# Kernel tuning notes

Measured on AMD Instinct MI355X. Metric: run time of the kernel, lower is better.

## Reference

```python
import jax, jax.numpy as jnp
import numpy as np

C = 512
NUM_HEADS = 8
RF = 4          # reduction_factor
GROUPS = 8      # min(8, C//8)
EPS = 1e-5


def _pos_enc(h, w, c):
    # matches torch _create_positional_encoding; c must be divisible by 4
    y = jnp.arange(h, dtype=jnp.float32)[:, None] * jnp.ones((1, w), jnp.float32)
    x = jnp.ones((h, 1), jnp.float32) * jnp.arange(w, dtype=jnp.float32)[None, :]
    div = jnp.exp(jnp.arange(0, c // 2, 2, dtype=jnp.float32) * (-np.log(10000.0) / (c // 2)))  # [c//4]
    d = div[:, None, None]
    sy, cy = jnp.sin(y[None] * d), jnp.cos(y[None] * d)   # [c//4,h,w]
    sx, cx = jnp.sin(x[None] * d), jnp.cos(x[None] * d)
    pe = jnp.stack([sy, cy, sx, cx], axis=1).reshape(c, h, w)  # interleaved 0::4..3::4
    return pe[None] * 0.01


def _group_norm(x, w, b):
    B, Cc, H, W = x.shape
    g = x.reshape(B, GROUPS, -1)
    m = g.mean(-1, keepdims=True)
    v = g.var(-1, keepdims=True)
    g = (g - m) / jnp.sqrt(v + EPS)
    return g.reshape(B, Cc, H, W) * w[None, :, None, None] + b[None, :, None, None]


def setup_inputs() -> dict:
    key = jax.random.key(0)
    ks = jax.random.split(key, 4)
    B, H, W = 1, 256, 256
    x = jax.random.normal(ks[0], (B, C, H, W), jnp.float32)
    qkv_w = jax.random.normal(ks[1], (3 * C, C), jnp.float32) * 0.02
    proj_w = jax.random.normal(ks[2], (C, C), jnp.float32) * 0.02
    gamma = jax.random.normal(ks[3], (1,), jnp.float32)
    return {
        "x": x,
        "gn_weight": jnp.ones((C,), jnp.float32),
        "gn_bias": jnp.zeros((C,), jnp.float32),
        "qkv_w": qkv_w,
        "proj_w": proj_w,
        "proj_b": jnp.zeros((C,), jnp.float32),
        "gamma": gamma,
        "temperature": jnp.ones((NUM_HEADS, 1, 1), jnp.float32),
    }


def reference(x, gn_weight, gn_bias, qkv_w, proj_w, proj_b, gamma, temperature):
    B, Cc, H, W = x.shape
    hd = Cc // NUM_HEADS
    identity = x
    xn = _group_norm(x, gn_weight, gn_bias)
    # spatial reduction (AvgPool2d k=4 s=4); H,W > 32 in this config
    Hr, Wr = H // RF, W // RF
    xr = xn.reshape(B, Cc, Hr, RF, Wr, RF).mean(axis=(3, 5))
    xr = xr + _pos_enc(Hr, Wr, Cc)
    qkv = jnp.einsum('oc,bchw->bohw', qkv_w, xr)  # 1x1 conv, no bias
    q, k, v = jnp.split(qkv, 3, axis=1)
    N = Hr * Wr
    q = q.reshape(B, NUM_HEADS, hd, N) * (hd ** -0.5) * temperature[None]
    k = k.reshape(B, NUM_HEADS, hd, N)
    v = v.reshape(B, NUM_HEADS, hd, N)
    # chunked attention in torch == plain softmax attention (chunking over queries)
    attn = jax.nn.softmax(jnp.einsum('bhdn,bhdm->bhnm', q, k), axis=-1)
    out = jnp.einsum('bhnm,bhdm->bhdn', attn, v).reshape(B, Cc, Hr, Wr)
    out = jax.image.resize(out, (B, Cc, H, W), method='bilinear')  # align_corners=False
    out = jnp.einsum('oc,bchw->bohw', proj_w, out) + proj_b[None, :, None, None]
    # dropout in eval mode is identity
    return identity + gamma * out
```

## Files before the change

### kernel.cpp

```cpp
#include <hip/hip_runtime.h>
#include <hip/hip_bf16.h>


typedef __attribute__((ext_vector_type(4))) short short4v;
typedef __attribute__((ext_vector_type(8))) short short8v;
typedef __attribute__((ext_vector_type(4))) float f32x4;
typedef __attribute__((ext_vector_type(4))) unsigned int u32x4;

#define MFMA16(a, b, c) __builtin_amdgcn_mfma_f32_16x16x32_bf16(a, b, c, 0, 0, 0)

__device__ __forceinline__ unsigned short bf16r(float f) {
    unsigned int u = __builtin_bit_cast(unsigned int, f);
    u += 0x7fffu + ((u >> 16) & 1u);
    return (unsigned short)(u >> 16);
}
__device__ __forceinline__ float bff(unsigned short s) {
    unsigned int u = ((unsigned int)s) << 16;
    return __builtin_bit_cast(float, u);
}
__device__ __forceinline__ unsigned int fbits(float f) {
    return __builtin_bit_cast(unsigned int, f);
}

typedef const __attribute__((address_space(1))) unsigned int guint;
typedef __attribute__((address_space(3))) unsigned int luint;
__device__ __forceinline__ void gload16(const void* g, void* l) {
    __builtin_amdgcn_global_load_lds((guint*)g, (luint*)l, 16, 0, 0);
}

__global__ __launch_bounds__(256) void k_wconv(const float* __restrict__ qkv_w,
                                               const float* __restrict__ proj_w,
                                               const float* __restrict__ temp,
                                               unsigned short* __restrict__ wq_b,
                                               unsigned short* __restrict__ wp_b) {
    int idx = blockIdx.x * 256 + threadIdx.x;
    const int NQ = 1536 * 512;
    if (idx < NQ) {
        int o = idx >> 9;
        float sc = (o < 512) ? temp[o >> 6] * 0.125f * 1.44269504f : 1.0f;
        wq_b[idx] = bf16r(qkv_w[idx] * sc);
    } else {
        int j = idx - NQ;
        wp_b[j] = bf16r(proj_w[j]);
    }
}

__global__ __launch_bounds__(256) void k_pool(const float* __restrict__ x,
                                              float* __restrict__ xp,
                                              float* __restrict__ partials) {
    int hr = blockIdx.x;
    int c  = blockIdx.y;
    int t = threadIdx.x;
    int r = t >> 6, wq = t & 63;
    const float4* src = (const float4*)(x + (size_t)c * 65536 + (size_t)(4 * hr + r) * 256 + 4 * wq);
    float4 v = *src;
    float s4 = v.x + v.y + v.z + v.w;
    float q4 = v.x * v.x + v.y * v.y + v.z * v.z + v.w * v.w;

    __shared__ float sm[256];
    __shared__ float wq4[4];
    sm[t] = s4;
    float qq = q4;
#pragma unroll
    for (int off = 1; off < 64; off <<= 1) qq += __shfl_xor(qq, off, 64);
    if ((t & 63) == 0) wq4[t >> 6] = qq;
    __syncthreads();
    if (t < 64) {
        float cs = sm[t] + sm[64 + t] + sm[128 + t] + sm[192 + t];
        xp[(size_t)c * 4096 + hr * 64 + t] = cs * (1.0f / 16.0f);
        float ts = cs;
#pragma unroll
        for (int off = 1; off < 64; off <<= 1) ts += __shfl_xor(ts, off, 64);
        if (t == 0) {
            int g = c >> 6;
            int slot = (c & 63) * 64 + hr;
            partials[(size_t)(g * 4096 + slot) * 2 + 0] = ts;
            partials[(size_t)(g * 4096 + slot) * 2 + 1] = wq4[0] + wq4[1] + wq4[2] + wq4[3];
        }
    }
}

__global__ __launch_bounds__(256) void k_stats(const float* __restrict__ partials,
                                               float* __restrict__ gstats) {
    int g = blockIdx.x;
    int t = threadIdx.x;
    float s = 0.f, q = 0.f;
    for (int i = t; i < 4096; i += 256) {
        s += partials[(size_t)(g * 4096 + i) * 2 + 0];
        q += partials[(size_t)(g * 4096 + i) * 2 + 1];
    }
#pragma unroll
    for (int off = 1; off < 64; off <<= 1) {
        s += __shfl_xor(s, off, 64);
        q += __shfl_xor(q, off, 64);
    }
    __shared__ float ss[4], qs[4];
    if ((t & 63) == 0) { ss[t >> 6] = s; qs[t >> 6] = q; }
    __syncthreads();
    if (t == 0) {
        float S = ss[0] + ss[1] + ss[2] + ss[3];
        float Q = qs[0] + qs[1] + qs[2] + qs[3];
        const float inv = 1.0f / 4194304.0f;
        float m = S * inv;
        float var = Q * inv - m * m;
        gstats[2 * g] = m;
        gstats[2 * g + 1] = rsqrtf(var + 1e-5f);
    }
}

__global__ __launch_bounds__(256) void k_xr(const float* __restrict__ xp,
                                            const float* __restrict__ gs,
                                            const float* __restrict__ gw,
                                            const float* __restrict__ gb,
                                            unsigned short* __restrict__ xr) {
    int idx = blockIdx.x * 256 + threadIdx.x;
    int c = idx >> 12, n = idx & 4095;
    int hr = n >> 6, wr = n & 63;
    int g = c >> 6;
    float m = gs[2 * g], rs = gs[2 * g + 1];
    float xn = (xp[idx] - m) * rs * gw[c] + gb[c];
    int i = c >> 2, kind = c & 3;
    float di = expf(-(float)i * 0.07195578415606394f);
    float arg = ((kind < 2) ? (float)hr : (float)wr) * di;
    float pe = 0.01f * ((kind & 1) ? cosf(arg) : sinf(arg));
    xr[idx] = bf16r(xn + pe);
}

__global__ __launch_bounds__(256) void k_gemm(const unsigned short* __restrict__ A,
                                              const unsigned short* __restrict__ B,
                                              unsigned short* __restrict__ C) {
    __shared__ unsigned short As[128][36];
    __shared__ unsigned short Bs[128][36];
    int t = threadIdx.x;
    int w = t >> 6, l = t & 63, l15 = l & 15, lg = l >> 4;
    int wrow = w >> 1, wcol = w & 1;
    int m0 = blockIdx.y * 128, n0 = blockIdx.x * 128;
    f32x4 acc[4][4] = {};

    for (int k0 = 0; k0 < 512; k0 += 32) {
#pragma unroll
        for (int i = 0; i < 4; i++) {
            int idx = t + 256 * i;
            int row = idx >> 3, kc = idx & 7;
            short4v av = *(const short4v*)(A + (size_t)(m0 + row) * 512 + k0 + 4 * kc);
            *(short4v*)&As[row][4 * kc] = av;
        }
#pragma unroll
        for (int i = 0; i < 4; i++) {
            int idx = t + 256 * i;
            int kr = idx >> 5, nc = idx & 31;
            short4v bv = *(const short4v*)(B + (size_t)(k0 + kr) * 4096 + n0 + 4 * nc);
#pragma unroll
            for (int j = 0; j < 4; j++) Bs[4 * nc + j][kr] = (unsigned short)bv[j];
        }
        __syncthreads();

        short8v af[4];
#pragma unroll
        for (int mi = 0; mi < 4; mi++) {
            int ar = wrow * 64 + mi * 16 + l15;
            short4v a0 = *(const short4v*)&As[ar][4 * lg];
            short4v a1 = *(const short4v*)&As[ar][16 + 4 * lg];
            af[mi] = __builtin_shufflevector(a0, a1, 0, 1, 2, 3, 4, 5, 6, 7);
        }
#pragma unroll
        for (int ni = 0; ni < 4; ni++) {
            int bc = wcol * 64 + ni * 16 + l15;
            short4v b0 = *(const short4v*)&Bs[bc][4 * lg];
            short4v b1 = *(const short4v*)&Bs[bc][16 + 4 * lg];
            short8v bf = __builtin_shufflevector(b0, b1, 0, 1, 2, 3, 4, 5, 6, 7);
#pragma unroll
            for (int mi = 0; mi < 4; mi++) acc[mi][ni] = MFMA16(af[mi], bf, acc[mi][ni]);
        }
        __syncthreads();
    }
#pragma unroll
    for (int mi = 0; mi < 4; mi++)
#pragma unroll
        for (int ni = 0; ni < 4; ni++) {
            int row = m0 + wrow * 64 + mi * 16 + 4 * lg;
            int col = n0 + wcol * 64 + ni * 16 + l15;
#pragma unroll
            for (int r = 0; r < 4; r++)
                C[(size_t)(row + r) * 4096 + col] = bf16r(acc[mi][ni][r]);
        }
}

__global__ __launch_bounds__(256) void k_perm(const unsigned short* __restrict__ qkv,
                                              unsigned short* __restrict__ qtg,
                                              unsigned short* __restrict__ ktg,
                                              unsigned short* __restrict__ vtg) {
    __shared__ unsigned short lt[64][72];
    int t = threadIdx.x;
    int tile = blockIdx.x, h = blockIdx.y, z = blockIdx.z;
    int base = (z == 0 ? 0 : (z == 1 ? 512 : 1024)) + h * 64;
#pragma unroll
    for (int i = 0; i < 2; i++) {
        int idx = t + 256 * i;
        int row = idx >> 3, sg = idx & 7;
        *(short8v*)&lt[row][sg * 8] =
            *(const short8v*)(qkv + (size_t)(base + row) * 4096 + tile * 64 + sg * 8);
    }
    __syncthreads();
#pragma unroll
    for (int i = 0; i < 2; i++) {
        int c = t + 256 * i;
        unsigned short o[8];
        unsigned short* dst;
        if (z == 0) {
            int nh = c >> 8, cl = c & 255;
            int s = cl >> 7, lgc = (cl >> 5) & 3, col = cl & 31;
#pragma unroll
            for (int j = 0; j < 4; j++) {
                o[j] = lt[s * 32 + 4 * lgc + j][nh * 32 + col];
                o[4 + j] = lt[s * 32 + 16 + 4 * lgc + j][nh * 32 + col];
            }
            dst = qtg + ((size_t)(h * 128 + tile * 2 + nh)) * 2048 + cl * 8;
        } else if (z == 1) {
            int s = c >> 8, lgc = (c >> 6) & 3, m = c & 63;
#pragma unroll
            for (int j = 0; j < 4; j++) {
                o[j] = lt[s * 32 + 4 * lgc + j][m];
                o[4 + j] = lt[s * 32 + 16 + 4 * lgc + j][m];
            }
            dst = ktg + ((size_t)(h * 64 + tile)) * 4096 + c * 8;
        } else {
            int mh = c >> 8, lgc = (c >> 6) & 3, d = c & 63;
#pragma unroll
            for (int j = 0; j < 4; j++) {
                o[j] = lt[d][mh * 32 + 4 * lgc + j];
                o[4 + j] = lt[d][mh * 32 + 16 + 4 * lgc + j];
            }
            dst = vtg + ((size_t)(h * 64 + tile)) * 4096 + c * 8;
        }
        *(short8v*)dst = *(const short8v*)o;
    }
}

__global__ __launch_bounds__(512, 4) void k_attn(const unsigned short* __restrict__ qtg,
                                                 const unsigned short* __restrict__ ktg,
                                                 const unsigned short* __restrict__ vtg,
                                                 unsigned short* __restrict__ opart,
                                                 float* __restrict__ lgl) {
    __shared__ __align__(16) unsigned short kbuf[3][4096];
    __shared__ __align__(16) unsigned short vbuf[3][4096];
    int t = threadIdx.x;
    int l = t & 63, l15 = l & 15, lg = l >> 4, w = t >> 6;
    int qt = blockIdx.x, h = blockIdx.y, seg = blockIdx.z;
    int nu = qt * 8 + w;

    const unsigned short* qb = qtg + ((size_t)(h * 128 + nu)) * 2048;
    const unsigned short* kb = ktg + ((size_t)(h * 64 + seg * 8)) * 4096;
    const unsigned short* vb = vtg + ((size_t)(h * 64 + seg * 8)) * 4096;

    short8v qf[2][2];
#pragma unroll
    for (int ng = 0; ng < 2; ng++)
#pragma unroll
        for (int s = 0; s < 2; s++)
            qf[ng][s] = *(const short8v*)(qb + ((s * 4 + lg) * 32 + ng * 16 + l15) * 8);

    int st = t & 255;
    const unsigned short* sp = ((t >= 256) ? vb : kb) + st * 8;
    unsigned short* ld0 = ((t >= 256) ? &vbuf[0][0] : &kbuf[0][0]) + st * 8;

    f32x4 od[2][4] = {};
    float lsum[2] = {0.f, 0.f};

#define STAGE(kt, b)                                      \
    {                                                     \
        gload16(sp + (kt) * 4096, ld0 + (b) * 4096);      \
        gload16(sp + (kt) * 4096 + 2048, ld0 + (b) * 4096 + 2048); \
    }

    STAGE(0, 0);
    STAGE(1, 1);

    int cur = 0, nxt = 2;
#pragma unroll 1
    for (int j = 0; j < 8; j++) {
        if (j < 7) {
            asm volatile("s_waitcnt vmcnt(2)" ::: "memory");
        } else {
            asm volatile("s_waitcnt vmcnt(0)" ::: "memory");
        }
        __builtin_amdgcn_s_barrier();
        __builtin_amdgcn_sched_barrier(0);
        if (j < 6) STAGE(j + 2, nxt);

        const unsigned short* kl = &kbuf[0][0] + cur * 4096;
        const unsigned short* vl = &vbuf[0][0] + cur * 4096;

        short8v pb[2][2];
        float p[2][2][4];
#pragma unroll
        for (int mf = 0; mf < 4; mf++) {
            short8v k0 = *(const short8v*)(kl + ((0 + lg) * 64 + mf * 16 + l15) * 8);
            short8v k1 = *(const short8v*)(kl + ((4 + lg) * 64 + mf * 16 + l15) * 8);
            f32x4 s0 = {}, s1 = {};
            __builtin_amdgcn_s_setprio(1);
            s0 = MFMA16(k0, qf[0][0], s0);
            s0 = MFMA16(k1, qf[0][1], s0);
            s1 = MFMA16(k0, qf[1][0], s1);
            s1 = MFMA16(k1, qf[1][1], s1);
            __builtin_amdgcn_s_setprio(0);
            int half = mf & 1;
#pragma unroll
            for (int r = 0; r < 4; r++) {
                p[0][half][r] = __builtin_amdgcn_exp2f(s0[r]);
                p[1][half][r] = __builtin_amdgcn_exp2f(s1[r]);
            }
            lsum[0] += (p[0][half][0] + p[0][half][1]) + (p[0][half][2] + p[0][half][3]);
            lsum[1] += (p[1][half][0] + p[1][half][1]) + (p[1][half][2] + p[1][half][3]);
            if (half) {
                int mh = mf >> 1;
#pragma unroll
                for (int ng = 0; ng < 2; ng++) {
                    u32x4 P;
                    P[0] = __builtin_amdgcn_perm(fbits(p[ng][0][1]), fbits(p[ng][0][0]), 0x07060302u);
                    P[1] = __builtin_amdgcn_perm(fbits(p[ng][0][3]), fbits(p[ng][0][2]), 0x07060302u);
                    P[2] = __builtin_amdgcn_perm(fbits(p[ng][1][1]), fbits(p[ng][1][0]), 0x07060302u);
                    P[3] = __builtin_amdgcn_perm(fbits(p[ng][1][3]), fbits(p[ng][1][2]), 0x07060302u);
                    pb[ng][mh] = __builtin_bit_cast(short8v, P);
                }
            }
        }

        __builtin_amdgcn_s_setprio(1);
#pragma unroll
        for (int mh = 0; mh < 2; mh++)
#pragma unroll
            for (int dg = 0; dg < 4; dg++) {
                short8v vf = *(const short8v*)(vl + ((mh * 4 + lg) * 64 + dg * 16 + l15) * 8);
                od[0][dg] = MFMA16(vf, pb[0][mh], od[0][dg]);
                od[1][dg] = MFMA16(vf, pb[1][mh], od[1][dg]);
            }
        __builtin_amdgcn_s_setprio(0);

        cur = (cur == 2) ? 0 : cur + 1;
        nxt = (nxt == 2) ? 0 : nxt + 1;
    }
#undef STAGE

#pragma unroll
    for (int ng = 0; ng < 2; ng++) {
        lsum[ng] += __shfl_xor(lsum[ng], 16, 64);
        lsum[ng] += __shfl_xor(lsum[ng], 32, 64);
    }

    unsigned short* op = opart + ((size_t)(seg * 512 + h * 64)) * 4096 + nu * 32;
#pragma unroll
    for (int ng = 0; ng < 2; ng++)
#pragma unroll
        for (int dg = 0; dg < 4; dg++)
#pragma unroll
            for (int r = 0; r < 4; r++) {
                int d = dg * 16 + 4 * lg + r;
                op[(size_t)d * 4096 + ng * 16 + l15] = bf16r(od[ng][dg][r]);
            }
    if (lg == 0) {
#pragma unroll
        for (int ng = 0; ng < 2; ng++)
            lgl[(size_t)(seg * 8 + h) * 4096 + nu * 32 + ng * 16 + l15] = lsum[ng];
    }
}

__global__ __launch_bounds__(256) void k_merge(const unsigned short* __restrict__ opart,
                                               const float* __restrict__ lgl,
                                               unsigned short* __restrict__ attn_b) {
    int bid = blockIdx.x, t = threadIdx.x;
    int row = bid >> 2;
    int n0 = (bid & 3) * 1024 + t * 4;
    int h = row >> 6;

    f32x4 den = {};
    float num[4] = {};
#pragma unroll
    for (int s = 0; s < 8; s++) {
        f32x4 lv = *(const f32x4*)(lgl + (size_t)(s * 8 + h) * 4096 + n0);
        den += lv;
        short4v ov = *(const short4v*)(opart + (size_t)s * 2097152 + (size_t)row * 4096 + n0);
#pragma unroll
        for (int j = 0; j < 4; j++) num[j] += bff((unsigned short)ov[j]);
    }
    unsigned short res[4];
#pragma unroll
    for (int j = 0; j < 4; j++) res[j] = bf16r(num[j] / den[j]);
    *(short4v*)(attn_b + (size_t)row * 4096 + n0) = *(const short4v*)res;
}

__global__ __launch_bounds__(256) void k_up(const float* __restrict__ x,
                                            const unsigned short* __restrict__ low,
                                            const float* __restrict__ proj_b,
                                            const float* __restrict__ gamma,
                                            float* __restrict__ out) {
    int t = threadIdx.x;
    int hs = t >> 6;
    int hh = blockIdx.x * 4 + hs;
    int c = blockIdx.y;
    int a = t & 63;

    int ph = hh & 3, Ah = hh >> 2;
    int y0 = Ah + ((ph < 2) ? -1 : 0);
    float fy = (ph < 2) ? (0.625f + 0.25f * ph) : (0.125f + 0.25f * (ph - 2));
    int y1 = min(y0 + 1, 63); y0 = max(y0, 0);

    const unsigned short* L0 = low + (size_t)c * 4096 + y0 * 64;
    const unsigned short* L1 = low + (size_t)c * 4096 + y1 * 64;
    int am = max(a - 1, 0), ap = min(a + 1, 63);
    float gy = 1.f - fy;
    float vm = gy * bff(L0[am]) + fy * bff(L1[am]);
    float v0 = gy * bff(L0[a])  + fy * bff(L1[a]);
    float vp = gy * bff(L0[ap]) + fy * bff(L1[ap]);

    float pb = proj_b[c], g = gamma[0];
    size_t idx = (size_t)c * 65536 + (size_t)hh * 256 + a * 4;
    float4 xi = *(const float4*)(x + idx);
    float4 o;
    o.x = xi.x + g * (0.375f * vm + 0.625f * v0 + pb);
    o.y = xi.y + g * (0.125f * vm + 0.875f * v0 + pb);
    o.z = xi.z + g * (0.875f * v0 + 0.125f * vp + pb);
    o.w = xi.w + g * (0.625f * v0 + 0.375f * vp + pb);
    *(float4*)(out + idx) = o;
}

extern "C" void kernel_launch(void* const* d_in, const int* in_sizes, int n_in,
                              void* d_out, int out_size, void* d_ws, size_t ws_size,
                              hipStream_t stream) {
    const float* x     = (const float*)d_in[0];
    const float* gnw   = (const float*)d_in[1];
    const float* gnb   = (const float*)d_in[2];
    const float* qkvw  = (const float*)d_in[3];
    const float* projw = (const float*)d_in[4];
    const float* projb = (const float*)d_in[5];
    const float* gamma = (const float*)d_in[6];
    const float* temp  = (const float*)d_in[7];

    char* ws = (char*)d_ws;
    const size_t MB = 1u << 20;
    float* gstats          = (float*)(ws + 0);
    float* partials        = (float*)(ws + 1024);
    float* xp              = (float*)(ws + 1 * MB);
    unsigned short* qtg    = (unsigned short*)(ws + 1 * MB);
    unsigned short* ktg    = (unsigned short*)(ws + 5 * MB);
    unsigned short* xr_b   = (unsigned short*)(ws + 9 * MB);
    unsigned short* vtg    = (unsigned short*)(ws + 9 * MB);
    unsigned short* wq_b   = (unsigned short*)(ws + 13 * MB);
    unsigned short* wp_b   = (unsigned short*)(ws + 15 * MB);
    unsigned short* qkv_b  = (unsigned short*)(ws + 16 * MB);
    unsigned short* attn_b = (unsigned short*)(ws + 28 * MB);
    unsigned short* low_b  = (unsigned short*)(ws + 32 * MB);
    float* out = (float*)d_out;
    unsigned short* opart = (unsigned short*)d_out;
    float* lgl = (float*)((char*)d_out + 32 * MB);

    k_wconv<<<4096, 256, 0, stream>>>(qkvw, projw, temp, wq_b, wp_b);
    k_pool<<<dim3(64, 512), 256, 0, stream>>>(x, xp, partials);
    k_stats<<<8, 256, 0, stream>>>(partials, gstats);
    k_xr<<<8192, 256, 0, stream>>>(xp, gstats, gnw, gnb, xr_b);
    k_gemm<<<dim3(32, 12), 256, 0, stream>>>(wq_b, xr_b, qkv_b);
    k_perm<<<dim3(64, 8, 3), 256, 0, stream>>>(qkv_b, qtg, ktg, vtg);
    k_attn<<<dim3(16, 8, 8), 512, 0, stream>>>(qtg, ktg, vtg, opart, lgl);
    k_merge<<<2048, 256, 0, stream>>>(opart, lgl, attn_b);
    k_gemm<<<dim3(32, 4), 256, 0, stream>>>(wp_b, attn_b, low_b);
    k_up<<<dim3(64, 512), 256, 0, stream>>>(x, low_b, projb, gamma, out);
}
```

Before: 190.0 us.

## Fold weight conversion into pool, shrink attention blocks, transpose merge output layout

Weight conversion to bf16 now runs as extra blocks of the pooling kernel, which removes one launch. The attention kernel drops from 512-thread blocks with triple buffering to 256-thread blocks with double buffering and an extra barrier per iteration, giving more blocks per CU. Partial outputs are written in a per-query contiguous layout, so the merge kernel can use wide vector loads and write a transposed attention matrix. A new GEMM variant reads that transposed matrix as its B operand. The risk is less load-ahead in the attention pipeline and the extra synchronisation each iteration.

```diff
diff --git a/kernel.cpp b/kernel.cpp
--- a/kernel.cpp
+++ b/kernel.cpp
@@ -28,26 +28,27 @@
     __builtin_amdgcn_global_load_lds((guint*)g, (luint*)l, 16, 0, 0);
 }
 
-__global__ __launch_bounds__(256) void k_wconv(const float* __restrict__ qkv_w,
-                                               const float* __restrict__ proj_w,
-                                               const float* __restrict__ temp,
-                                               unsigned short* __restrict__ wq_b,
-                                               unsigned short* __restrict__ wp_b) {
-    int idx = blockIdx.x * 256 + threadIdx.x;
-    const int NQ = 1536 * 512;
-    if (idx < NQ) {
-        int o = idx >> 9;
-        float sc = (o < 512) ? temp[o >> 6] * 0.125f * 1.44269504f : 1.0f;
-        wq_b[idx] = bf16r(qkv_w[idx] * sc);
-    } else {
-        int j = idx - NQ;
-        wp_b[j] = bf16r(proj_w[j]);
-    }
-}
-
 __global__ __launch_bounds__(256) void k_pool(const float* __restrict__ x,
                                               float* __restrict__ xp,
-                                              float* __restrict__ partials) {
+                                              float* __restrict__ partials,
+                                              const float* __restrict__ qkv_w,
+                                              const float* __restrict__ proj_w,
+                                              const float* __restrict__ temp,
+                                              unsigned short* __restrict__ wq_b,
+                                              unsigned short* __restrict__ wp_b) {
+    if (blockIdx.x >= 64) {
+        int idx = ((blockIdx.x - 64) * 512 + blockIdx.y) * 256 + threadIdx.x;
+        const int NQ = 1536 * 512;
+        const int NTOT = NQ + 512 * 512;
+        if (idx < NQ) {
+            int o = idx >> 9;
+            float sc = (o < 512) ? temp[o >> 6] * 0.125f * 1.44269504f : 1.0f;
+            wq_b[idx] = bf16r(qkv_w[idx] * sc);
+        } else if (idx < NTOT) {
+            wp_b[idx - NQ] = bf16r(proj_w[idx - NQ]);
+        }
+        return;
+    }
     int hr = blockIdx.x;
     int c  = blockIdx.y;
     int t = threadIdx.x;
@@ -186,6 +187,60 @@
         }
 }
 
+__global__ __launch_bounds__(256) void k_gemmT(const unsigned short* __restrict__ A,
+                                               const unsigned short* __restrict__ BT,
+                                               unsigned short* __restrict__ C) {
+    __shared__ unsigned short As[128][36];
+    __shared__ unsigned short Bs[128][36];
+    int t = threadIdx.x;
+    int w = t >> 6, l = t & 63, l15 = l & 15, lg = l >> 4;
+    int wrow = w >> 1, wcol = w & 1;
+    int m0 = blockIdx.y * 128, n0 = blockIdx.x * 128;
+    f32x4 acc[4][4] = {};
+
+    for (int k0 = 0; k0 < 512; k0 += 32) {
+#pragma unroll
+        for (int i = 0; i < 4; i++) {
+            int idx = t + 256 * i;
+            int row = idx >> 3, kc = idx & 7;
+            short4v av = *(const short4v*)(A + (size_t)(m0 + row) * 512 + k0 + 4 * kc);
+            *(short4v*)&As[row][4 * kc] = av;
+            short4v bv = *(const short4v*)(BT + (size_t)(n0 + row) * 512 + k0 + 4 * kc);
+            *(short4v*)&Bs[row][4 * kc] = bv;
+        }
+        __syncthreads();
+
+        short8v af[4];
+#pragma unroll
+        for (int mi = 0; mi < 4; mi++) {
+            int ar = wrow * 64 + mi * 16 + l15;
+            short4v a0 = *(const short4v*)&As[ar][4 * lg];
+            short4v a1 = *(const short4v*)&As[ar][16 + 4 * lg];
+            af[mi] = __builtin_shufflevector(a0, a1, 0, 1, 2, 3, 4, 5, 6, 7);
+        }
+#pragma unroll
+        for (int ni = 0; ni < 4; ni++) {
+            int bc = wcol * 64 + ni * 16 + l15;
+            short4v b0 = *(const short4v*)&Bs[bc][4 * lg];
+            short4v b1 = *(const short4v*)&Bs[bc][16 + 4 * lg];
+            short8v bf = __builtin_shufflevector(b0, b1, 0, 1, 2, 3, 4, 5, 6, 7);
+#pragma unroll
+            for (int mi = 0; mi < 4; mi++) acc[mi][ni] = MFMA16(af[mi], bf, acc[mi][ni]);
+        }
+        __syncthreads();
+    }
+#pragma unroll
+    for (int mi = 0; mi < 4; mi++)
+#pragma unroll
+        for (int ni = 0; ni < 4; ni++) {
+            int row = m0 + wrow * 64 + mi * 16 + 4 * lg;
+            int col = n0 + wcol * 64 + ni * 16 + l15;
+#pragma unroll
+            for (int r = 0; r < 4; r++)
+                C[(size_t)(row + r) * 4096 + col] = bf16r(acc[mi][ni][r]);
+        }
+}
+
 __global__ __launch_bounds__(256) void k_perm(const unsigned short* __restrict__ qkv,
                                               unsigned short* __restrict__ qtg,
                                               unsigned short* __restrict__ ktg,
@@ -237,17 +292,17 @@
     }
 }
 
-__global__ __launch_bounds__(512, 4) void k_attn(const unsigned short* __restrict__ qtg,
+__global__ __launch_bounds__(256, 5) void k_attn(const unsigned short* __restrict__ qtg,
                                                  const unsigned short* __restrict__ ktg,
                                                  const unsigned short* __restrict__ vtg,
                                                  unsigned short* __restrict__ opart,
                                                  float* __restrict__ lgl) {
-    __shared__ __align__(16) unsigned short kbuf[3][4096];
-    __shared__ __align__(16) unsigned short vbuf[3][4096];
+    __shared__ __align__(16) unsigned short kbuf[2][4096];
+    __shared__ __align__(16) unsigned short vbuf[2][4096];
     int t = threadIdx.x;
     int l = t & 63, l15 = l & 15, lg = l >> 4, w = t >> 6;
     int qt = blockIdx.x, h = blockIdx.y, seg = blockIdx.z;
-    int nu = qt * 8 + w;
+    int nu = qt * 4 + w;
 
     const unsigned short* qb = qtg + ((size_t)(h * 128 + nu)) * 2048;
     const unsigned short* kb = ktg + ((size_t)(h * 64 + seg * 8)) * 4096;
@@ -260,39 +315,36 @@
         for (int s = 0; s < 2; s++)
             qf[ng][s] = *(const short8v*)(qb + ((s * 4 + lg) * 32 + ng * 16 + l15) * 8);
 
-    int st = t & 255;
-    const unsigned short* sp = ((t >= 256) ? vb : kb) + st * 8;
-    unsigned short* ld0 = ((t >= 256) ? &vbuf[0][0] : &kbuf[0][0]) + st * 8;
-
     f32x4 od[2][4] = {};
     float lsum[2] = {0.f, 0.f};
 
-#define STAGE(kt, b)                                      \
-    {                                                     \
-        gload16(sp + (kt) * 4096, ld0 + (b) * 4096);      \
-        gload16(sp + (kt) * 4096 + 2048, ld0 + (b) * 4096 + 2048); \
+#define STAGE(kt, b)                                                            \
+    {                                                                           \
+        gload16(kb + (size_t)(kt) * 4096 + t * 8, &kbuf[b][t * 8]);             \
+        gload16(kb + (size_t)(kt) * 4096 + (t + 256) * 8, &kbuf[b][(t + 256) * 8]); \
+        gload16(vb + (size_t)(kt) * 4096 + t * 8, &vbuf[b][t * 8]);             \
+        gload16(vb + (size_t)(kt) * 4096 + (t + 256) * 8, &vbuf[b][(t + 256) * 8]); \
     }
 
     STAGE(0, 0);
-    STAGE(1, 1);
-
-    int cur = 0, nxt = 2;
+
+    int u = 0;
 #pragma unroll 1
     for (int j = 0; j < 8; j++) {
         if (j < 7) {
-            asm volatile("s_waitcnt vmcnt(2)" ::: "memory");
+            STAGE(j + 1, u ^ 1);
+            asm volatile("s_waitcnt vmcnt(4)" ::: "memory");
         } else {
             asm volatile("s_waitcnt vmcnt(0)" ::: "memory");
         }
         __builtin_amdgcn_s_barrier();
         __builtin_amdgcn_sched_barrier(0);
-        if (j < 6) STAGE(j + 2, nxt);
-
-        const unsigned short* kl = &kbuf[0][0] + cur * 4096;
-        const unsigned short* vl = &vbuf[0][0] + cur * 4096;
-
+
+        const unsigned short* kl = &kbuf[u][0];
+        const unsigned short* vl = &vbuf[u][0];
+
+        u32x4 pwA, pwB;
         short8v pb[2][2];
-        float p[2][2][4];
 #pragma unroll
         for (int mf = 0; mf < 4; mf++) {
             short8v k0 = *(const short8v*)(kl + ((0 + lg) * 64 + mf * 16 + l15) * 8);
@@ -304,25 +356,26 @@
             s1 = MFMA16(k0, qf[1][0], s1);
             s1 = MFMA16(k1, qf[1][1], s1);
             __builtin_amdgcn_s_setprio(0);
-            int half = mf & 1;
+            float p0[4], p1[4];
 #pragma unroll
             for (int r = 0; r < 4; r++) {
-                p[0][half][r] = __builtin_amdgcn_exp2f(s0[r]);
-                p[1][half][r] = __builtin_amdgcn_exp2f(s1[r]);
+                p0[r] = __builtin_amdgcn_exp2f(s0[r]);
+                p1[r] = __builtin_amdgcn_exp2f(s1[r]);
             }
-            lsum[0] += (p[0][half][0] + p[0][half][1]) + (p[0][half][2] + p[0][half][3]);
-            lsum[1] += (p[1][half][0] + p[1][half][1]) + (p[1][half][2] + p[1][half][3]);
-            if (half) {
-                int mh = mf >> 1;
-#pragma unroll
-                for (int ng = 0; ng < 2; ng++) {
-                    u32x4 P;
-                    P[0] = __builtin_amdgcn_perm(fbits(p[ng][0][1]), fbits(p[ng][0][0]), 0x07060302u);
-                    P[1] = __builtin_amdgcn_perm(fbits(p[ng][0][3]), fbits(p[ng][0][2]), 0x07060302u);
-                    P[2] = __builtin_amdgcn_perm(fbits(p[ng][1][1]), fbits(p[ng][1][0]), 0x07060302u);
-                    P[3] = __builtin_amdgcn_perm(fbits(p[ng][1][3]), fbits(p[ng][1][2]), 0x07060302u);
-                    pb[ng][mh] = __builtin_bit_cast(short8v, P);
-                }
+            lsum[0] += (p0[0] + p0[1]) + (p0[2] + p0[3]);
+            lsum[1] += (p1[0] + p1[1]) + (p1[2] + p1[3]);
+            if (!(mf & 1)) {
+                pwA[0] = __builtin_amdgcn_perm(fbits(p0[1]), fbits(p0[0]), 0x07060302u);
+                pwA[1] = __builtin_amdgcn_perm(fbits(p0[3]), fbits(p0[2]), 0x07060302u);
+                pwB[0] = __builtin_amdgcn_perm(fbits(p1[1]), fbits(p1[0]), 0x07060302u);
+                pwB[1] = __builtin_amdgcn_perm(fbits(p1[3]), fbits(p1[2]), 0x07060302u);
+            } else {
+                pwA[2] = __builtin_amdgcn_perm(fbits(p0[1]), fbits(p0[0]), 0x07060302u);
+                pwA[3] = __builtin_amdgcn_perm(fbits(p0[3]), fbits(p0[2]), 0x07060302u);
+                pwB[2] = __builtin_amdgcn_perm(fbits(p1[1]), fbits(p1[0]), 0x07060302u);
+                pwB[3] = __builtin_amdgcn_perm(fbits(p1[3]), fbits(p1[2]), 0x07060302u);
+                pb[0][mf >> 1] = __builtin_bit_cast(short8v, pwA);
+                pb[1][mf >> 1] = __builtin_bit_cast(short8v, pwB);
             }
         }
 
@@ -337,8 +390,8 @@
             }
         __builtin_amdgcn_s_setprio(0);
 
-        cur = (cur == 2) ? 0 : cur + 1;
-        nxt = (nxt == 2) ? 0 : nxt + 1;
+        __builtin_amdgcn_s_barrier();
+        u ^= 1;
     }
 #undef STAGE
 
@@ -348,16 +401,16 @@
         lsum[ng] += __shfl_xor(lsum[ng], 32, 64);
     }
 
-    unsigned short* op = opart + ((size_t)(seg * 512 + h * 64)) * 4096 + nu * 32;
+    unsigned short* op = opart + (((size_t)(seg * 8 + h)) * 4096 + nu * 32) * 64;
 #pragma unroll
     for (int ng = 0; ng < 2; ng++)
 #pragma unroll
-        for (int dg = 0; dg < 4; dg++)
-#pragma unroll
-            for (int r = 0; r < 4; r++) {
-                int d = dg * 16 + 4 * lg + r;
-                op[(size_t)d * 4096 + ng * 16 + l15] = bf16r(od[ng][dg][r]);
-            }
+        for (int dg = 0; dg < 4; dg++) {
+            unsigned short v4[4];
+#pragma unroll
+            for (int r = 0; r < 4; r++) v4[r] = bf16r(od[ng][dg][r]);
+            *(short4v*)(op + (ng * 16 + l15) * 64 + dg * 16 + 4 * lg) = *(const short4v*)v4;
+        }
     if (lg == 0) {
 #pragma unroll
         for (int ng = 0; ng < 2; ng++)
@@ -367,26 +420,33 @@
 
 __global__ __launch_bounds__(256) void k_merge(const unsigned short* __restrict__ opart,
                                                const float* __restrict__ lgl,
-                                               unsigned short* __restrict__ attn_b) {
-    int bid = blockIdx.x, t = threadIdx.x;
-    int row = bid >> 2;
-    int n0 = (bid & 3) * 1024 + t * 4;
-    int h = row >> 6;
-
-    f32x4 den = {};
-    float num[4] = {};
+                                               unsigned short* __restrict__ attn_bT) {
+    int t = threadIdx.x;
+    int n = blockIdx.x * 8 + (t >> 5);
+    int cid = t & 31;
+    int h = cid >> 2, d0 = (cid & 3) * 16;
+
+    float den = 0.f;
+    float num[16] = {};
 #pragma unroll
     for (int s = 0; s < 8; s++) {
-        f32x4 lv = *(const f32x4*)(lgl + (size_t)(s * 8 + h) * 4096 + n0);
-        den += lv;
-        short4v ov = *(const short4v*)(opart + (size_t)s * 2097152 + (size_t)row * 4096 + n0);
-#pragma unroll
-        for (int j = 0; j < 4; j++) num[j] += bff((unsigned short)ov[j]);
-    }
-    unsigned short res[4];
-#pragma unroll
-    for (int j = 0; j < 4; j++) res[j] = bf16r(num[j] / den[j]);
-    *(short4v*)(attn_b + (size_t)row * 4096 + n0) = *(const short4v*)res;
+        den += lgl[(size_t)(s * 8 + h) * 4096 + n];
+        const unsigned short* row = opart + (((size_t)(s * 8 + h)) * 4096 + n) * 64 + d0;
+        short8v a = *(const short8v*)row;
+        short8v b = *(const short8v*)(row + 8);
+#pragma unroll
+        for (int j = 0; j < 8; j++) {
+            num[j] += bff((unsigned short)a[j]);
+            num[8 + j] += bff((unsigned short)b[j]);
+        }
+    }
+    float inv = 1.0f / den;
+    unsigned short res[16];
+#pragma unroll
+    for (int j = 0; j < 16; j++) res[j] = bf16r(num[j] * inv);
+    unsigned short* dst = attn_bT + (size_t)n * 512 + h * 64 + d0;
+    *(short8v*)dst = *(const short8v*)&res[0];
+    *(short8v*)(dst + 8) = *(const short8v*)&res[8];
 }
 
 __global__ __launch_bounds__(256) void k_up(const float* __restrict__ x,
@@ -448,20 +508,19 @@
     unsigned short* wq_b   = (unsigned short*)(ws + 13 * MB);
     unsigned short* wp_b   = (unsigned short*)(ws + 15 * MB);
     unsigned short* qkv_b  = (unsigned short*)(ws + 16 * MB);
-    unsigned short* attn_b = (unsigned short*)(ws + 28 * MB);
+    unsigned short* attn_bT= (unsigned short*)(ws + 28 * MB);
     unsigned short* low_b  = (unsigned short*)(ws + 32 * MB);
     float* out = (float*)d_out;
     unsigned short* opart = (unsigned short*)d_out;
-    float* lgl = (float*)((char*)d_out + 32 * MB);
-
-    k_wconv<<<4096, 256, 0, stream>>>(qkvw, projw, temp, wq_b, wp_b);
-    k_pool<<<dim3(64, 512), 256, 0, stream>>>(x, xp, partials);
+    float* lgl = (float*)((char*)d_out + 40 * MB);
+
+    k_pool<<<dim3(72, 512), 256, 0, stream>>>(x, xp, partials, qkvw, projw, temp, wq_b, wp_b);
     k_stats<<<8, 256, 0, stream>>>(partials, gstats);
     k_xr<<<8192, 256, 0, stream>>>(xp, gstats, gnw, gnb, xr_b);
     k_gemm<<<dim3(32, 12), 256, 0, stream>>>(wq_b, xr_b, qkv_b);
     k_perm<<<dim3(64, 8, 3), 256, 0, stream>>>(qkv_b, qtg, ktg, vtg);
-    k_attn<<<dim3(16, 8, 8), 512, 0, stream>>>(qtg, ktg, vtg, opart, lgl);
-    k_merge<<<2048, 256, 0, stream>>>(opart, lgl, attn_b);
-    k_gemm<<<dim3(32, 4), 256, 0, stream>>>(wp_b, attn_b, low_b);
+    k_attn<<<dim3(32, 8, 8), 256, 0, stream>>>(qtg, ktg, vtg, opart, lgl);
+    k_merge<<<512, 256, 0, stream>>>(opart, lgl, attn_bT);
+    k_gemmT<<<dim3(32, 4), 256, 0, stream>>>(wp_b, attn_bT, low_b);
     k_up<<<dim3(64, 512), 256, 0, stream>>>(x, low_b, projb, gamma, out);
 }
```

After: 185.6 us. -2.3%, faster.
